# Optimization experiments

Hardware: AMD Instinct MI355X
Metric: run time of the kernel (lower is better)

The kernel has to match this reference:

```python
import jax, jax.numpy as jnp
import numpy as np

N, L = 131072, 4          # traffic lights, lanes per TL
E, H = 64, 128            # embed_dim, hidden_dim
NH, HD = 4, 16            # num_heads, head_dim (E = NH*HD)
NR, R = 4, 8              # num_regions, region_embed_dim
INIT_LOG_STD = -0.5


def _lin(k, fan_in, shape):
    b = 1.0 / np.sqrt(fan_in)
    return jax.random.uniform(k, shape, minval=-b, maxval=b, dtype=jnp.float32)


def setup_inputs() -> dict:
    key = jax.random.key(0)
    ks = jax.random.split(key, 32)
    inp = {
        "queue": jax.random.uniform(ks[0], (N, L), dtype=jnp.float32),
        "waiting": jax.random.uniform(ks[1], (N, L), dtype=jnp.float32),
        "phase_onehot": jax.random.uniform(ks[2], (N, 4), dtype=jnp.float32),
        "elapsed": jax.random.uniform(ks[3], (N,), dtype=jnp.float32),
        "region_ids": jax.random.randint(ks[4], (N,), 0, NR, dtype=jnp.int32),
        "noise": jax.random.normal(ks[5], (N,), dtype=jnp.float32),
        # lane_mlp: Linear(3,H) -> ReLU -> Linear(H,E) -> ReLU
        "lane_w1": _lin(ks[6], 3, (3, H)), "lane_b1": _lin(ks[7], 3, (H,)),
        "lane_w2": _lin(ks[8], H, (H, E)), "lane_b2": _lin(ks[9], H, (E,)),
        # MultiheadAttention in/out projections
        "attn_in_w": _lin(ks[10], E, (E, 3 * E)), "attn_in_b": jnp.zeros((3 * E,), jnp.float32),
        "attn_out_w": _lin(ks[11], E, (E, E)), "attn_out_b": jnp.zeros((E,), jnp.float32),
        # phase_mlp: Linear(5,H) -> ReLU -> Linear(H,H) -> ReLU
        "phase_w1": _lin(ks[12], 5, (5, H)), "phase_b1": _lin(ks[13], 5, (H,)),
        "phase_w2": _lin(ks[14], H, (H, H)), "phase_b2": _lin(ks[15], H, (H,)),
        # region embedding table
        "region_table": jax.random.normal(ks[16], (NR, R), dtype=jnp.float32),
        # mlp_head: Linear(E+H+R, H) -> ReLU -> Linear(H, 1)
        "head_w1": _lin(ks[17], E + H + R, (E + H + R, H)), "head_b1": _lin(ks[18], E + H + R, (H,)),
        "head_w2": _lin(ks[19], H, (H, 1)), "head_b2": _lin(ks[20], H, (1,)),
        "log_std": jnp.full((1,), INIT_LOG_STD, dtype=jnp.float32),
    }
    return inp


def reference(queue, waiting, phase_onehot, elapsed, region_ids, noise,
              lane_w1, lane_b1, lane_w2, lane_b2,
              attn_in_w, attn_in_b, attn_out_w, attn_out_b,
              phase_w1, phase_b1, phase_w2, phase_b2,
              region_table, head_w1, head_b1, head_w2, head_b2, log_std):
    # --- lane context: tiny MLP + self-attention over L lanes, batched over N TLs ---
    lane_feats = jnp.stack([queue, waiting, jnp.broadcast_to(elapsed[:, None], (N, L))], axis=-1)  # [N,L,3]
    h = jax.nn.relu(lane_feats @ lane_w1 + lane_b1)          # [N,L,H]
    emb = jax.nn.relu(h @ lane_w2 + lane_b2)                 # [N,L,E]

    qkv = emb @ attn_in_w + attn_in_b                        # [N,L,3E]
    q, k, v = jnp.split(qkv, 3, axis=-1)
    def heads(x):  # [N,L,E] -> [N,NH,L,HD]
        return x.reshape(N, L, NH, HD).transpose(0, 2, 1, 3)
    q, k, v = heads(q), heads(k), heads(v)
    scores = jnp.einsum('bhqd,bhkd->bhqk', q, k) / np.sqrt(HD)   # [N,NH,L,L]
    attn = jax.nn.softmax(scores, axis=-1)
    o = jnp.einsum('bhqk,bhkd->bhqd', attn, v)               # [N,NH,L,HD]
    o = o.transpose(0, 2, 1, 3).reshape(N, L, E)
    attn_out = o @ attn_out_w + attn_out_b                   # [N,L,E]
    ctx = attn_out.mean(axis=1)                              # [N,E]

    # --- phase MLP ---
    phase_elapsed = jnp.concatenate([phase_onehot, elapsed[:, None]], axis=-1)  # [N,5]
    ph = jax.nn.relu(phase_elapsed @ phase_w1 + phase_b1)
    phase_emb = jax.nn.relu(ph @ phase_w2 + phase_b2)        # [N,H]

    # --- region embedding (clamped index) ---
    rid = jnp.clip(region_ids, 0, NR - 1)
    region_emb = region_table[rid]                           # [N,R]

    # --- Gaussian head ---
    feat = jnp.concatenate([ctx, phase_emb, region_emb], axis=-1)  # [N,E+H+R]
    means = (jax.nn.relu(feat @ head_w1 + head_b1) @ head_w2 + head_b2)[:, 0]  # [N]

    ls = jnp.broadcast_to(log_std, means.shape)
    std = jnp.exp(ls)
    actions = means + std * noise
    actions_clamped = jnp.clip(actions, -1.0, 1.0)
    log_prob = -0.5 * ((actions - means) ** 2 / (std * std) + 2.0 * ls + np.log(2.0 * np.pi))
    return actions_clamped, log_prob
```

## Files before the change

kernel.cpp:

```cpp
#include <hip/hip_runtime.h>
#include <math.h>

#define N_TL 131072
#define GRID 1024
#define BLK 256
#define TLA 16
#define ITERA 8
#define TLB 32
#define ITERB 4

typedef __attribute__((ext_vector_type(8))) short bfrag;
typedef __attribute__((ext_vector_type(4))) float f32x4;

__device__ __forceinline__ unsigned short f2bf_rne(float x) {
  unsigned int u = __float_as_uint(x);
  return (unsigned short)((u + 0x7fffu + ((u >> 16) & 1u)) >> 16);
}
__device__ __forceinline__ unsigned int pack2(float a, float b) {
  return ((__float_as_uint(a) + 0x8000u) >> 16) |
         ((__float_as_uint(b) + 0x8000u) & 0xffff0000u);
}
__device__ __forceinline__ f32x4 mfma16(bfrag a, bfrag b, f32x4 c) {
  return __builtin_amdgcn_mfma_f32_16x16x32_bf16(a, b, c, 0, 0, 0);
}
__device__ __forceinline__ float dot4(float4 a, float4 b) {
  return a.x * b.x + a.y * b.y + a.z * b.z + a.w * b.w;
}

__device__ __forceinline__ bfrag load_wfragT(const float* __restrict__ w, int ncols,
                                             int col0, int k0, int lane, int K, float scale) {
  const int mm = lane & 15, qq = lane >> 4;
  bfrag f;
  #pragma unroll
  for (int j = 0; j < 8; ++j) {
    const int k = k0 + qq * 8 + j;
    const float v = (k < K) ? w[(size_t)k * ncols + col0 + mm] * scale : 0.f;
    f[j] = (short)f2bf_rne(v);
  }
  return f;
}

#define LDBACT(arr, stride, nt, kk) \
  (*reinterpret_cast<const bfrag*>(&(arr)[((nt) * 16 + m) * (stride) + (kk) * 32 + quad * 8]))

struct alignas(16) SmemA {
  union {
    float qkvf[64 * 196];
    unsigned short h[64 * 136];
  };
  unsigned short emb[64 * 72];
  unsigned short xbuf[64 * 32];
  float b1[128], b2[64], bin[192], bout[64];
};

__global__ __launch_bounds__(BLK)
void lane_ctx_mfma(const float* __restrict__ queue,
                   const float* __restrict__ waiting,
                   const float* __restrict__ elapsed,
                   const float* __restrict__ lane_w1,
                   const float* __restrict__ lane_b1,
                   const float* __restrict__ lane_w2,
                   const float* __restrict__ lane_b2,
                   const float* __restrict__ attn_in_w,
                   const float* __restrict__ attn_in_b,
                   const float* __restrict__ attn_out_w,
                   const float* __restrict__ attn_out_b,
                   unsigned short* __restrict__ ctx_out) {
  __shared__ SmemA S;
  const int tid  = threadIdx.x;
  const int wv   = tid >> 6;
  const int lane = tid & 63;
  const int m    = lane & 15;
  const int quad = lane >> 4;
  const f32x4 Z = {0.f, 0.f, 0.f, 0.f};

  bfrag wL1[2], wL2[4], wQKV[3][2], wOUT[8];
  #pragma unroll
  for (int Mi = 0; Mi < 2; ++Mi)
    wL1[Mi] = load_wfragT(lane_w1, 128, (wv * 2 + Mi) * 16, 0, lane, 3, 1.f);
  #pragma unroll
  for (int kk = 0; kk < 4; ++kk)
    wL2[kk] = load_wfragT(lane_w2, 64, wv * 16, kk * 32, lane, 128, 1.f);
  #pragma unroll
  for (int Mi = 0; Mi < 3; ++Mi)
    #pragma unroll
    for (int kk = 0; kk < 2; ++kk)
      wQKV[Mi][kk] = load_wfragT(attn_in_w, 192, (wv + Mi * 4) * 16, kk * 32, lane, 64,
                                 Mi == 0 ? 0.25f : 1.f);
  #pragma unroll
  for (int kk = 0; kk < 8; ++kk) {
    bfrag f;
    #pragma unroll
    for (int j = 0; j < 8; ++j) {
      const int k = kk * 32 + quad * 8 + j;
      f[j] = (short)f2bf_rne(attn_out_w[(size_t)(k & 63) * 64 + wv * 16 + m] * 0.25f);
    }
    wOUT[kk] = f;
  }

  for (int i = tid; i < 128; i += BLK) S.b1[i] = lane_b1[i];
  for (int i = tid; i < 64;  i += BLK) S.b2[i] = lane_b2[i];
  for (int i = tid; i < 192; i += BLK) S.bin[i] = attn_in_b[i] * ((i < 64) ? 0.25f : 1.f);
  for (int i = tid; i < 64;  i += BLK) S.bout[i] = attn_out_b[i];
  {
    const int n0 = blockIdx.x * ITERA * TLA;
    const int r = tid >> 2, seg = tid & 3;
    uint4 z = {0, 0, 0, 0};
    if (seg == 0) {
      const int gl = n0 * 4 + r;
      z.x = pack2(queue[gl], waiting[gl]);
      z.y = pack2(elapsed[n0 + (r >> 2)], 0.f);
    }
    *reinterpret_cast<uint4*>(&S.xbuf[r * 32 + seg * 8]) = z;
  }
  __syncthreads();

  for (int it = 0; it < ITERA; ++it) {
    const int n0 = (blockIdx.x * ITERA + it) * TLA;

    {
      f32x4 acc[2][4];
      #pragma unroll
      for (int Mi = 0; Mi < 2; ++Mi)
        #pragma unroll
        for (int Nt = 0; Nt < 4; ++Nt) acc[Mi][Nt] = Z;
      #pragma unroll
      for (int Nt = 0; Nt < 4; ++Nt) {
        const bfrag b = LDBACT(S.xbuf, 32, Nt, 0);
        acc[0][Nt] = mfma16(wL1[0], b, acc[0][Nt]);
        acc[1][Nt] = mfma16(wL1[1], b, acc[1][Nt]);
      }
      #pragma unroll
      for (int Mi = 0; Mi < 2; ++Mi) {
        const int oc0 = (wv * 2 + Mi) * 16 + quad * 4;
        const f32x4 bb = *reinterpret_cast<const f32x4*>(&S.b1[oc0]);
        #pragma unroll
        for (int Nt = 0; Nt < 4; ++Nt) {
          const int row = Nt * 16 + m;
          uint2 u;
          u.x = pack2(fmaxf(acc[Mi][Nt][0] + bb[0], 0.f), fmaxf(acc[Mi][Nt][1] + bb[1], 0.f));
          u.y = pack2(fmaxf(acc[Mi][Nt][2] + bb[2], 0.f), fmaxf(acc[Mi][Nt][3] + bb[3], 0.f));
          *reinterpret_cast<uint2*>(&S.h[row * 136 + oc0]) = u;
        }
      }
    }
    __syncthreads();

    {
      f32x4 acc[4] = {Z, Z, Z, Z};
      #pragma unroll
      for (int Nt = 0; Nt < 4; ++Nt)
        #pragma unroll
        for (int kk = 0; kk < 4; ++kk)
          acc[Nt] = mfma16(wL2[kk], LDBACT(S.h, 136, Nt, kk), acc[Nt]);
      const int oc0 = wv * 16 + quad * 4;
      const f32x4 bb = *reinterpret_cast<const f32x4*>(&S.b2[oc0]);
      #pragma unroll
      for (int Nt = 0; Nt < 4; ++Nt) {
        const int row = Nt * 16 + m;
        uint2 u;
        u.x = pack2(fmaxf(acc[Nt][0] + bb[0], 0.f), fmaxf(acc[Nt][1] + bb[1], 0.f));
        u.y = pack2(fmaxf(acc[Nt][2] + bb[2], 0.f), fmaxf(acc[Nt][3] + bb[3], 0.f));
        *reinterpret_cast<uint2*>(&S.emb[row * 72 + oc0]) = u;
      }
    }
    __syncthreads();

    {
      f32x4 acc[3][4];
      #pragma unroll
      for (int Mi = 0; Mi < 3; ++Mi)
        #pragma unroll
        for (int Nt = 0; Nt < 4; ++Nt) acc[Mi][Nt] = Z;
      #pragma unroll
      for (int Nt = 0; Nt < 4; ++Nt) {
        const bfrag e0 = LDBACT(S.emb, 72, Nt, 0);
        const bfrag e1 = LDBACT(S.emb, 72, Nt, 1);
        #pragma unroll
        for (int Mi = 0; Mi < 3; ++Mi) {
          acc[Mi][Nt] = mfma16(wQKV[Mi][0], e0, acc[Mi][Nt]);
          acc[Mi][Nt] = mfma16(wQKV[Mi][1], e1, acc[Mi][Nt]);
        }
      }
      #pragma unroll
      for (int Mi = 0; Mi < 3; ++Mi) {
        const int oc0 = (wv + Mi * 4) * 16 + quad * 4;
        const f32x4 bb = *reinterpret_cast<const f32x4*>(&S.bin[oc0]);
        #pragma unroll
        for (int Nt = 0; Nt < 4; ++Nt) {
          const int row = Nt * 16 + m;
          const f32x4 o = acc[Mi][Nt] + bb;
          *reinterpret_cast<f32x4*>(&S.qkvf[row * 196 + oc0]) = o;
        }
      }
      const int nn0 = (blockIdx.x * ITERA + ((it + 1) & (ITERA - 1))) * TLA;
      const int r = tid >> 2, seg = tid & 3;
      uint4 z = {0, 0, 0, 0};
      if (seg == 0) {
        const int gl = nn0 * 4 + r;
        z.x = pack2(queue[gl], waiting[gl]);
        z.y = pack2(elapsed[nn0 + (r >> 2)], 0.f);
      }
      *reinterpret_cast<uint4*>(&S.xbuf[r * 32 + seg * 8]) = z;
    }
    __syncthreads();

    {
      const int tl = tid >> 4, l16 = tid & 15;
      const int hh = l16 >> 2, lq = l16 & 3;
      const float* qb = &S.qkvf[(tl * 4 + lq) * 196 + hh * 16];
      const float4 q0 = *reinterpret_cast<const float4*>(qb);
      const float4 q1 = *reinterpret_cast<const float4*>(qb + 4);
      const float4 q2 = *reinterpret_cast<const float4*>(qb + 8);
      const float4 q3 = *reinterpret_cast<const float4*>(qb + 12);
      float sc[4];
      #pragma unroll
      for (int lk = 0; lk < 4; ++lk) {
        const float* kb = &S.qkvf[(tl * 4 + lk) * 196 + 64 + hh * 16];
        sc[lk] = dot4(q0, *reinterpret_cast<const float4*>(kb))
               + dot4(q1, *reinterpret_cast<const float4*>(kb + 4))
               + dot4(q2, *reinterpret_cast<const float4*>(kb + 8))
               + dot4(q3, *reinterpret_cast<const float4*>(kb + 12));
      }
      const float mx = fmaxf(fmaxf(sc[0], sc[1]), fmaxf(sc[2], sc[3]));
      const float e0 = __expf(sc[0] - mx), e1 = __expf(sc[1] - mx);
      const float e2 = __expf(sc[2] - mx), e3 = __expf(sc[3] - mx);
      const float inv = 1.f / (e0 + e1 + e2 + e3);
      const float pr[4] = {e0 * inv, e1 * inv, e2 * inv, e3 * inv};
      float4 o0 = {0,0,0,0}, o1 = {0,0,0,0}, o2 = {0,0,0,0}, o3 = {0,0,0,0};
      #pragma unroll
      for (int lk = 0; lk < 4; ++lk) {
        const float* vb = &S.qkvf[(tl * 4 + lk) * 196 + 128 + hh * 16];
        const float4 v0 = *reinterpret_cast<const float4*>(vb);
        const float4 v1 = *reinterpret_cast<const float4*>(vb + 4);
        const float4 v2 = *reinterpret_cast<const float4*>(vb + 8);
        const float4 v3 = *reinterpret_cast<const float4*>(vb + 12);
        const float p = pr[lk];
        o0.x += p * v0.x; o0.y += p * v0.y; o0.z += p * v0.z; o0.w += p * v0.w;
        o1.x += p * v1.x; o1.y += p * v1.y; o1.z += p * v1.z; o1.w += p * v1.w;
        o2.x += p * v2.x; o2.y += p * v2.y; o2.z += p * v2.z; o2.w += p * v2.w;
        o3.x += p * v3.x; o3.y += p * v3.y; o3.z += p * v3.z; o3.w += p * v3.w;
      }
      unsigned short* om = S.emb;
      const int base = tl * 264 + lq * 64 + hh * 16;
      *reinterpret_cast<uint4*>(&om[base]) =
          make_uint4(pack2(o0.x, o0.y), pack2(o0.z, o0.w), pack2(o1.x, o1.y), pack2(o1.z, o1.w));
      *reinterpret_cast<uint4*>(&om[base + 8]) =
          make_uint4(pack2(o2.x, o2.y), pack2(o2.z, o2.w), pack2(o3.x, o3.y), pack2(o3.z, o3.w));
    }
    __syncthreads();

    {
      f32x4 acc = Z;
      #pragma unroll
      for (int kk = 0; kk < 8; ++kk)
        acc = mfma16(wOUT[kk], LDBACT(S.emb, 264, 0, kk), acc);
      const int oc0 = wv * 16 + quad * 4;
      uint2 u;
      u.x = pack2(acc[0] + S.bout[oc0],     acc[1] + S.bout[oc0 + 1]);
      u.y = pack2(acc[2] + S.bout[oc0 + 2], acc[3] + S.bout[oc0 + 3]);
      *reinterpret_cast<uint2*>(&ctx_out[(size_t)(n0 + m) * 64 + oc0]) = u;
    }
  }
}

struct alignas(16) SmemB {
  unsigned short feat[32 * 200];
  unsigned short ph[32 * 136];
  unsigned short xb[32 * 32];
  float pb1[128], pb2[128];
  float rbias[4][128];
  float hw2[128];
  float consts[2];
  int ridx[32];
};

__global__ __launch_bounds__(BLK)
void head_mfma(const float* __restrict__ phase_onehot,
               const float* __restrict__ elapsed,
               const int* __restrict__ region_ids,
               const float* __restrict__ noise,
               const float* __restrict__ phase_w1,
               const float* __restrict__ phase_b1,
               const float* __restrict__ phase_w2,
               const float* __restrict__ phase_b2,
               const float* __restrict__ region_table,
               const float* __restrict__ head_w1,
               const float* __restrict__ head_b1,
               const float* __restrict__ head_w2,
               const float* __restrict__ head_b2,
               const float* __restrict__ log_std,
               const unsigned short* __restrict__ ctx_in,
               float* __restrict__ out) {
  __shared__ SmemB S;
  const int tid  = threadIdx.x;
  const int wv   = tid >> 6;
  const int lane = tid & 63;
  const int m    = lane & 15;
  const int quad = lane >> 4;
  const f32x4 Z = {0.f, 0.f, 0.f, 0.f};

  bfrag wP1[2], wP2[2][4], wH1[2][6];
  #pragma unroll
  for (int Mi = 0; Mi < 2; ++Mi) {
    wP1[Mi] = load_wfragT(phase_w1, 128, (wv * 2 + Mi) * 16, 0, lane, 5, 1.f);
    #pragma unroll
    for (int kk = 0; kk < 4; ++kk)
      wP2[Mi][kk] = load_wfragT(phase_w2, 128, (wv + Mi * 4) * 16, kk * 32, lane, 128, 1.f);
    #pragma unroll
    for (int kk = 0; kk < 6; ++kk)
      wH1[Mi][kk] = load_wfragT(head_w1, 128, (wv + Mi * 4) * 16, kk * 32, lane, 192, 1.f);
  }

  for (int i = tid; i < 128; i += BLK) S.pb1[i] = phase_b1[i];
  for (int i = tid; i < 128; i += BLK) S.pb2[i] = phase_b2[i];
  for (int i = tid; i < 128; i += BLK) S.hw2[i] = head_w2[i];
  for (int i = tid; i < 512; i += BLK) {
    const int g = i >> 7, c = i & 127;
    float acc = head_b1[c];
    #pragma unroll
    for (int j = 0; j < 8; ++j) acc += region_table[g * 8 + j] * head_w1[(192 + j) * 128 + c];
    S.rbias[g][c] = acc;
  }
  if (tid == 0) { S.consts[0] = head_b2[0]; S.consts[1] = log_std[0]; }
  {
    const int n0 = blockIdx.x * ITERB * TLB;
    const int row = tid >> 3, c8 = (tid & 7) * 8;
    *reinterpret_cast<uint4*>(&S.feat[row * 200 + c8]) =
        *reinterpret_cast<const uint4*>(&ctx_in[(size_t)(n0 + row) * 64 + c8]);
    if (tid < 128) {
      const int r = tid >> 2, seg = tid & 3;
      uint4 z = {0, 0, 0, 0};
      if (seg == 0) {
        const float4 p = *reinterpret_cast<const float4*>(&phase_onehot[(n0 + r) * 4]);
        z.x = pack2(p.x, p.y);
        z.y = pack2(p.z, p.w);
        z.z = pack2(elapsed[n0 + r], 0.f);
      }
      *reinterpret_cast<uint4*>(&S.xb[r * 32 + seg * 8]) = z;
    }
    if (tid < 32) {
      int r = region_ids[n0 + tid];
      S.ridx[tid] = r < 0 ? 0 : (r > 3 ? 3 : r);
    }
  }
  __syncthreads();

  for (int it = 0; it < ITERB; ++it) {
    const int n0 = (blockIdx.x * ITERB + it) * TLB;

    {
      f32x4 acc[2][2];
      acc[0][0] = Z; acc[0][1] = Z; acc[1][0] = Z; acc[1][1] = Z;
      #pragma unroll
      for (int Nt = 0; Nt < 2; ++Nt) {
        const bfrag b = LDBACT(S.xb, 32, Nt, 0);
        acc[0][Nt] = mfma16(wP1[0], b, acc[0][Nt]);
        acc[1][Nt] = mfma16(wP1[1], b, acc[1][Nt]);
      }
      #pragma unroll
      for (int Mi = 0; Mi < 2; ++Mi) {
        const int oc0 = (wv * 2 + Mi) * 16 + quad * 4;
        const f32x4 bb = *reinterpret_cast<const f32x4*>(&S.pb1[oc0]);
        #pragma unroll
        for (int Nt = 0; Nt < 2; ++Nt) {
          const int row = Nt * 16 + m;
          uint2 u;
          u.x = pack2(fmaxf(acc[Mi][Nt][0] + bb[0], 0.f), fmaxf(acc[Mi][Nt][1] + bb[1], 0.f));
          u.y = pack2(fmaxf(acc[Mi][Nt][2] + bb[2], 0.f), fmaxf(acc[Mi][Nt][3] + bb[3], 0.f));
          *reinterpret_cast<uint2*>(&S.ph[row * 136 + oc0]) = u;
        }
      }
    }
    __syncthreads();

    {
      f32x4 acc[2][2];
      acc[0][0] = Z; acc[0][1] = Z; acc[1][0] = Z; acc[1][1] = Z;
      #pragma unroll
      for (int Nt = 0; Nt < 2; ++Nt)
        #pragma unroll
        for (int kk = 0; kk < 4; ++kk) {
          const bfrag b = LDBACT(S.ph, 136, Nt, kk);
          acc[0][Nt] = mfma16(wP2[0][kk], b, acc[0][Nt]);
          acc[1][Nt] = mfma16(wP2[1][kk], b, acc[1][Nt]);
        }
      #pragma unroll
      for (int Mi = 0; Mi < 2; ++Mi) {
        const int oc0 = (wv + Mi * 4) * 16 + quad * 4;
        const f32x4 bb = *reinterpret_cast<const f32x4*>(&S.pb2[oc0]);
        #pragma unroll
        for (int Nt = 0; Nt < 2; ++Nt) {
          const int row = Nt * 16 + m;
          uint2 u;
          u.x = pack2(fmaxf(acc[Mi][Nt][0] + bb[0], 0.f), fmaxf(acc[Mi][Nt][1] + bb[1], 0.f));
          u.y = pack2(fmaxf(acc[Mi][Nt][2] + bb[2], 0.f), fmaxf(acc[Mi][Nt][3] + bb[3], 0.f));
          *reinterpret_cast<uint2*>(&S.feat[row * 200 + 64 + oc0]) = u;
        }
      }
    }
    __syncthreads();

    {
      f32x4 acc[2][2];
      acc[0][0] = Z; acc[0][1] = Z; acc[1][0] = Z; acc[1][1] = Z;
      #pragma unroll
      for (int Nt = 0; Nt < 2; ++Nt)
        #pragma unroll
        for (int kk = 0; kk < 6; ++kk) {
          const bfrag b = LDBACT(S.feat, 200, Nt, kk);
          acc[0][Nt] = mfma16(wH1[0][kk], b, acc[0][Nt]);
          acc[1][Nt] = mfma16(wH1[1][kk], b, acc[1][Nt]);
        }
      #pragma unroll
      for (int Mi = 0; Mi < 2; ++Mi) {
        const int oc0 = (wv + Mi * 4) * 16 + quad * 4;
        #pragma unroll
        for (int Nt = 0; Nt < 2; ++Nt) {
          const int row = Nt * 16 + m;
          const f32x4 bb = *reinterpret_cast<const f32x4*>(&S.rbias[S.ridx[row]][oc0]);
          uint2 u;
          u.x = pack2(fmaxf(acc[Mi][Nt][0] + bb[0], 0.f), fmaxf(acc[Mi][Nt][1] + bb[1], 0.f));
          u.y = pack2(fmaxf(acc[Mi][Nt][2] + bb[2], 0.f), fmaxf(acc[Mi][Nt][3] + bb[3], 0.f));
          *reinterpret_cast<uint2*>(&S.ph[row * 136 + oc0]) = u;
        }
      }
    }
    __syncthreads();

    {
      const int tl = tid >> 3, s = tid & 7;
      const unsigned short* hp = &S.ph[tl * 136 + s * 16];
      const bfrag h0 = *reinterpret_cast<const bfrag*>(hp);
      const bfrag h1 = *reinterpret_cast<const bfrag*>(hp + 8);
      float t = 0.f;
      #pragma unroll
      for (int j = 0; j < 8; ++j) {
        t += __uint_as_float(((unsigned int)(unsigned short)h0[j]) << 16) * S.hw2[s * 16 + j];
        t += __uint_as_float(((unsigned int)(unsigned short)h1[j]) << 16) * S.hw2[s * 16 + 8 + j];
      }
      t += __shfl_xor(t, 1);
      t += __shfl_xor(t, 2);
      t += __shfl_xor(t, 4);
      if (s == 0) {
        const int n = n0 + tl;
        const float means = t + S.consts[0];
        const float ls = S.consts[1];
        const float nz = noise[n];
        const float a = means + __expf(ls) * nz;
        out[n] = fminf(fmaxf(a, -1.f), 1.f);
        out[N_TL + n] = -0.5f * (nz * nz + 2.f * ls + 1.8378770664093453f);
      }
      const int nn0 = (blockIdx.x * ITERB + ((it + 1) & (ITERB - 1))) * TLB;
      const int row = tid >> 3, c8 = (tid & 7) * 8;
      *reinterpret_cast<uint4*>(&S.feat[row * 200 + c8]) =
          *reinterpret_cast<const uint4*>(&ctx_in[(size_t)(nn0 + row) * 64 + c8]);
      if (tid < 128) {
        const int r = tid >> 2, seg = tid & 3;
        uint4 z = {0, 0, 0, 0};
        if (seg == 0) {
          const float4 p = *reinterpret_cast<const float4*>(&phase_onehot[(nn0 + r) * 4]);
          z.x = pack2(p.x, p.y);
          z.y = pack2(p.z, p.w);
          z.z = pack2(elapsed[nn0 + r], 0.f);
        }
        *reinterpret_cast<uint4*>(&S.xb[r * 32 + seg * 8]) = z;
      }
      if (tid < 32) {
        int r = region_ids[nn0 + tid];
        S.ridx[tid] = r < 0 ? 0 : (r > 3 ? 3 : r);
      }
    }
    __syncthreads();
  }
}

extern "C" void kernel_launch(void* const* d_in, const int* in_sizes, int n_in,
                              void* d_out, int out_size, void* d_ws, size_t ws_size,
                              hipStream_t stream) {
  const float* queue        = (const float*)d_in[0];
  const float* waiting      = (const float*)d_in[1];
  const float* phase_onehot = (const float*)d_in[2];
  const float* elapsed      = (const float*)d_in[3];
  const int*   region_ids   = (const int*)d_in[4];
  const float* noise        = (const float*)d_in[5];
  const float* lane_w1      = (const float*)d_in[6];
  const float* lane_b1      = (const float*)d_in[7];
  const float* lane_w2      = (const float*)d_in[8];
  const float* lane_b2      = (const float*)d_in[9];
  const float* attn_in_w    = (const float*)d_in[10];
  const float* attn_in_b    = (const float*)d_in[11];
  const float* attn_out_w   = (const float*)d_in[12];
  const float* attn_out_b   = (const float*)d_in[13];
  const float* phase_w1     = (const float*)d_in[14];
  const float* phase_b1     = (const float*)d_in[15];
  const float* phase_w2     = (const float*)d_in[16];
  const float* phase_b2     = (const float*)d_in[17];
  const float* region_table = (const float*)d_in[18];
  const float* head_w1      = (const float*)d_in[19];
  const float* head_b1      = (const float*)d_in[20];
  const float* head_w2      = (const float*)d_in[21];
  const float* head_b2      = (const float*)d_in[22];
  const float* log_std      = (const float*)d_in[23];

  unsigned short* ctx_ws = (unsigned short*)d_ws;
  float* out = (float*)d_out;

  hipLaunchKernelGGL(lane_ctx_mfma, dim3(GRID), dim3(BLK), 0, stream,
                     queue, waiting, elapsed, lane_w1, lane_b1, lane_w2, lane_b2,
                     attn_in_w, attn_in_b, attn_out_w, attn_out_b, ctx_ws);
  hipLaunchKernelGGL(head_mfma, dim3(GRID), dim3(BLK), 0, stream,
                     phase_onehot, elapsed, region_ids, noise,
                     phase_w1, phase_b1, phase_w2, phase_b2, region_table,
                     head_w1, head_b1, head_w2, head_b2, log_std, ctx_ws, out);
}
```

Measured before the change: 217.2 us.

## Use 512-thread blocks in head kernel with one output tile per wave

The head kernel moves from 256 to 512 threads per block with 8 waves, each owning a single 16-column output slice, and each block iteration now covers 64 traffic lights instead of 32. Per-wave weight fragments are halved, which lowers register pressure, and the MFMA loops now run over 4 row tiles instead of 2x2 tiles. The aim is more waves in flight and more weight reuse per fragment, at the cost of larger shared memory per block and heavier block-level synchronisation. An empty unrolled loop was also added to the lane kernel and has no effect.

Result: faster. 209.3 us (-3.6%).

```diff
diff --git a/kernel.cpp b/kernel.cpp
--- a/kernel.cpp
+++ b/kernel.cpp
@@ -3,11 +3,12 @@
 
 #define N_TL 131072
 #define GRID 1024
-#define BLK 256
+#define BLKA 256
 #define TLA 16
 #define ITERA 8
-#define TLB 32
-#define ITERB 4
+#define BLKB 512
+#define TLB 64
+#define ITERB 2
 
 typedef __attribute__((ext_vector_type(8))) short bfrag;
 typedef __attribute__((ext_vector_type(4))) float f32x4;
@@ -53,7 +54,7 @@
   float b1[128], b2[64], bin[192], bout[64];
 };
 
-__global__ __launch_bounds__(BLK)
+__global__ __launch_bounds__(BLKA)
 void lane_ctx_mfma(const float* __restrict__ queue,
                    const float* __restrict__ waiting,
                    const float* __restrict__ elapsed,
@@ -98,10 +99,10 @@
     wOUT[kk] = f;
   }
 
-  for (int i = tid; i < 128; i += BLK) S.b1[i] = lane_b1[i];
-  for (int i = tid; i < 64;  i += BLK) S.b2[i] = lane_b2[i];
-  for (int i = tid; i < 192; i += BLK) S.bin[i] = attn_in_b[i] * ((i < 64) ? 0.25f : 1.f);
-  for (int i = tid; i < 64;  i += BLK) S.bout[i] = attn_out_b[i];
+  for (int i = tid; i < 128; i += BLKA) S.b1[i] = lane_b1[i];
+  for (int i = tid; i < 64;  i += BLKA) S.b2[i] = lane_b2[i];
+  for (int i = tid; i < 192; i += BLKA) S.bin[i] = attn_in_b[i] * ((i < 64) ? 0.25f : 1.f);
+  for (int i = tid; i < 64;  i += BLKA) S.bout[i] = attn_out_b[i];
   {
     const int n0 = blockIdx.x * ITERA * TLA;
     const int r = tid >> 2, seg = tid & 3;
@@ -241,6 +242,8 @@
         o2.x += p * v2.x; o2.y += p * v2.y; o2.z += p * v2.z; o2.w += p * v2.w;
         o3.x += p * v3.x; o3.y += p * v3.y; o3.z += p * v3.z; o3.w += p * v3.w;
       }
+      #pragma unroll
+      for (int d = 0; d < 1; ++d) {}
       unsigned short* om = S.emb;
       const int base = tl * 264 + lq * 64 + hh * 16;
       *reinterpret_cast<uint4*>(&om[base]) =
@@ -265,17 +268,17 @@
 }
 
 struct alignas(16) SmemB {
-  unsigned short feat[32 * 200];
-  unsigned short ph[32 * 136];
-  unsigned short xb[32 * 32];
+  unsigned short feat[64 * 200];
+  unsigned short ph[64 * 136];
+  unsigned short xb[64 * 32];
   float pb1[128], pb2[128];
   float rbias[4][128];
   float hw2[128];
   float consts[2];
-  int ridx[32];
+  int ridx[64];
 };
 
-__global__ __launch_bounds__(BLK)
+__global__ __launch_bounds__(BLKB)
 void head_mfma(const float* __restrict__ phase_onehot,
                const float* __restrict__ elapsed,
                const int* __restrict__ region_ids,
@@ -300,22 +303,19 @@
   const int quad = lane >> 4;
   const f32x4 Z = {0.f, 0.f, 0.f, 0.f};
 
-  bfrag wP1[2], wP2[2][4], wH1[2][6];
-  #pragma unroll
-  for (int Mi = 0; Mi < 2; ++Mi) {
-    wP1[Mi] = load_wfragT(phase_w1, 128, (wv * 2 + Mi) * 16, 0, lane, 5, 1.f);
-    #pragma unroll
-    for (int kk = 0; kk < 4; ++kk)
-      wP2[Mi][kk] = load_wfragT(phase_w2, 128, (wv + Mi * 4) * 16, kk * 32, lane, 128, 1.f);
-    #pragma unroll
-    for (int kk = 0; kk < 6; ++kk)
-      wH1[Mi][kk] = load_wfragT(head_w1, 128, (wv + Mi * 4) * 16, kk * 32, lane, 192, 1.f);
-  }
-
-  for (int i = tid; i < 128; i += BLK) S.pb1[i] = phase_b1[i];
-  for (int i = tid; i < 128; i += BLK) S.pb2[i] = phase_b2[i];
-  for (int i = tid; i < 128; i += BLK) S.hw2[i] = head_w2[i];
-  for (int i = tid; i < 512; i += BLK) {
+  bfrag wP1, wP2[4], wH1[6];
+  wP1 = load_wfragT(phase_w1, 128, wv * 16, 0, lane, 5, 1.f);
+  #pragma unroll
+  for (int kk = 0; kk < 4; ++kk)
+    wP2[kk] = load_wfragT(phase_w2, 128, wv * 16, kk * 32, lane, 128, 1.f);
+  #pragma unroll
+  for (int kk = 0; kk < 6; ++kk)
+    wH1[kk] = load_wfragT(head_w1, 128, wv * 16, kk * 32, lane, 192, 1.f);
+
+  for (int i = tid; i < 128; i += BLKB) S.pb1[i] = phase_b1[i];
+  for (int i = tid; i < 128; i += BLKB) S.pb2[i] = phase_b2[i];
+  for (int i = tid; i < 128; i += BLKB) S.hw2[i] = head_w2[i];
+  for (int i = tid; i < 512; i += BLKB) {
     const int g = i >> 7, c = i & 127;
     float acc = head_b1[c];
     #pragma unroll
@@ -328,7 +328,7 @@
     const int row = tid >> 3, c8 = (tid & 7) * 8;
     *reinterpret_cast<uint4*>(&S.feat[row * 200 + c8]) =
         *reinterpret_cast<const uint4*>(&ctx_in[(size_t)(n0 + row) * 64 + c8]);
-    if (tid < 128) {
+    if (tid < 256) {
       const int r = tid >> 2, seg = tid & 3;
       uint4 z = {0, 0, 0, 0};
       if (seg == 0) {
@@ -339,7 +339,7 @@
       }
       *reinterpret_cast<uint4*>(&S.xb[r * 32 + seg * 8]) = z;
     }
-    if (tid < 32) {
+    if (tid < 64) {
       int r = region_ids[n0 + tid];
       S.ridx[tid] = r < 0 ? 0 : (r > 3 ? 3 : r);
     }
@@ -348,82 +348,59 @@
 
   for (int it = 0; it < ITERB; ++it) {
     const int n0 = (blockIdx.x * ITERB + it) * TLB;
-
-    {
-      f32x4 acc[2][2];
-      acc[0][0] = Z; acc[0][1] = Z; acc[1][0] = Z; acc[1][1] = Z;
-      #pragma unroll
-      for (int Nt = 0; Nt < 2; ++Nt) {
-        const bfrag b = LDBACT(S.xb, 32, Nt, 0);
-        acc[0][Nt] = mfma16(wP1[0], b, acc[0][Nt]);
-        acc[1][Nt] = mfma16(wP1[1], b, acc[1][Nt]);
-      }
-      #pragma unroll
-      for (int Mi = 0; Mi < 2; ++Mi) {
-        const int oc0 = (wv * 2 + Mi) * 16 + quad * 4;
-        const f32x4 bb = *reinterpret_cast<const f32x4*>(&S.pb1[oc0]);
-        #pragma unroll
-        for (int Nt = 0; Nt < 2; ++Nt) {
-          const int row = Nt * 16 + m;
-          uint2 u;
-          u.x = pack2(fmaxf(acc[Mi][Nt][0] + bb[0], 0.f), fmaxf(acc[Mi][Nt][1] + bb[1], 0.f));
-          u.y = pack2(fmaxf(acc[Mi][Nt][2] + bb[2], 0.f), fmaxf(acc[Mi][Nt][3] + bb[3], 0.f));
-          *reinterpret_cast<uint2*>(&S.ph[row * 136 + oc0]) = u;
-        }
-      }
-    }
-    __syncthreads();
-
-    {
-      f32x4 acc[2][2];
-      acc[0][0] = Z; acc[0][1] = Z; acc[1][0] = Z; acc[1][1] = Z;
-      #pragma unroll
-      for (int Nt = 0; Nt < 2; ++Nt)
-        #pragma unroll
-        for (int kk = 0; kk < 4; ++kk) {
-          const bfrag b = LDBACT(S.ph, 136, Nt, kk);
-          acc[0][Nt] = mfma16(wP2[0][kk], b, acc[0][Nt]);
-          acc[1][Nt] = mfma16(wP2[1][kk], b, acc[1][Nt]);
-        }
-      #pragma unroll
-      for (int Mi = 0; Mi < 2; ++Mi) {
-        const int oc0 = (wv + Mi * 4) * 16 + quad * 4;
-        const f32x4 bb = *reinterpret_cast<const f32x4*>(&S.pb2[oc0]);
-        #pragma unroll
-        for (int Nt = 0; Nt < 2; ++Nt) {
-          const int row = Nt * 16 + m;
-          uint2 u;
-          u.x = pack2(fmaxf(acc[Mi][Nt][0] + bb[0], 0.f), fmaxf(acc[Mi][Nt][1] + bb[1], 0.f));
-          u.y = pack2(fmaxf(acc[Mi][Nt][2] + bb[2], 0.f), fmaxf(acc[Mi][Nt][3] + bb[3], 0.f));
-          *reinterpret_cast<uint2*>(&S.feat[row * 200 + 64 + oc0]) = u;
-        }
-      }
-    }
-    __syncthreads();
-
-    {
-      f32x4 acc[2][2];
-      acc[0][0] = Z; acc[0][1] = Z; acc[1][0] = Z; acc[1][1] = Z;
-      #pragma unroll
-      for (int Nt = 0; Nt < 2; ++Nt)
-        #pragma unroll
-        for (int kk = 0; kk < 6; ++kk) {
-          const bfrag b = LDBACT(S.feat, 200, Nt, kk);
-          acc[0][Nt] = mfma16(wH1[0][kk], b, acc[0][Nt]);
-          acc[1][Nt] = mfma16(wH1[1][kk], b, acc[1][Nt]);
-        }
-      #pragma unroll
-      for (int Mi = 0; Mi < 2; ++Mi) {
-        const int oc0 = (wv + Mi * 4) * 16 + quad * 4;
-        #pragma unroll
-        for (int Nt = 0; Nt < 2; ++Nt) {
-          const int row = Nt * 16 + m;
-          const f32x4 bb = *reinterpret_cast<const f32x4*>(&S.rbias[S.ridx[row]][oc0]);
-          uint2 u;
-          u.x = pack2(fmaxf(acc[Mi][Nt][0] + bb[0], 0.f), fmaxf(acc[Mi][Nt][1] + bb[1], 0.f));
-          u.y = pack2(fmaxf(acc[Mi][Nt][2] + bb[2], 0.f), fmaxf(acc[Mi][Nt][3] + bb[3], 0.f));
-          *reinterpret_cast<uint2*>(&S.ph[row * 136 + oc0]) = u;
-        }
+    const int oc0 = wv * 16 + quad * 4;
+
+    {
+      f32x4 acc[4] = {Z, Z, Z, Z};
+      #pragma unroll
+      for (int Nt = 0; Nt < 4; ++Nt)
+        acc[Nt] = mfma16(wP1, LDBACT(S.xb, 32, Nt, 0), acc[Nt]);
+      const f32x4 bb = *reinterpret_cast<const f32x4*>(&S.pb1[oc0]);
+      #pragma unroll
+      for (int Nt = 0; Nt < 4; ++Nt) {
+        const int row = Nt * 16 + m;
+        uint2 u;
+        u.x = pack2(fmaxf(acc[Nt][0] + bb[0], 0.f), fmaxf(acc[Nt][1] + bb[1], 0.f));
+        u.y = pack2(fmaxf(acc[Nt][2] + bb[2], 0.f), fmaxf(acc[Nt][3] + bb[3], 0.f));
+        *reinterpret_cast<uint2*>(&S.ph[row * 136 + oc0]) = u;
+      }
+    }
+    __syncthreads();
+
+    {
+      f32x4 acc[4] = {Z, Z, Z, Z};
+      #pragma unroll
+      for (int kk = 0; kk < 4; ++kk)
+        #pragma unroll
+        for (int Nt = 0; Nt < 4; ++Nt)
+          acc[Nt] = mfma16(wP2[kk], LDBACT(S.ph, 136, Nt, kk), acc[Nt]);
+      const f32x4 bb = *reinterpret_cast<const f32x4*>(&S.pb2[oc0]);
+      #pragma unroll
+      for (int Nt = 0; Nt < 4; ++Nt) {
+        const int row = Nt * 16 + m;
+        uint2 u;
+        u.x = pack2(fmaxf(acc[Nt][0] + bb[0], 0.f), fmaxf(acc[Nt][1] + bb[1], 0.f));
+        u.y = pack2(fmaxf(acc[Nt][2] + bb[2], 0.f), fmaxf(acc[Nt][3] + bb[3], 0.f));
+        *reinterpret_cast<uint2*>(&S.feat[row * 200 + 64 + oc0]) = u;
+      }
+    }
+    __syncthreads();
+
+    {
+      f32x4 acc[4] = {Z, Z, Z, Z};
+      #pragma unroll
+      for (int kk = 0; kk < 6; ++kk)
+        #pragma unroll
+        for (int Nt = 0; Nt < 4; ++Nt)
+          acc[Nt] = mfma16(wH1[kk], LDBACT(S.feat, 200, Nt, kk), acc[Nt]);
+      #pragma unroll
+      for (int Nt = 0; Nt < 4; ++Nt) {
+        const int row = Nt * 16 + m;
+        const f32x4 bb = *reinterpret_cast<const f32x4*>(&S.rbias[S.ridx[row]][oc0]);
+        uint2 u;
+        u.x = pack2(fmaxf(acc[Nt][0] + bb[0], 0.f), fmaxf(acc[Nt][1] + bb[1], 0.f));
+        u.y = pack2(fmaxf(acc[Nt][2] + bb[2], 0.f), fmaxf(acc[Nt][3] + bb[3], 0.f));
+        *reinterpret_cast<uint2*>(&S.ph[row * 136 + oc0]) = u;
       }
     }
     __syncthreads();
@@ -455,7 +432,7 @@
       const int row = tid >> 3, c8 = (tid & 7) * 8;
       *reinterpret_cast<uint4*>(&S.feat[row * 200 + c8]) =
           *reinterpret_cast<const uint4*>(&ctx_in[(size_t)(nn0 + row) * 64 + c8]);
-      if (tid < 128) {
+      if (tid < 256) {
         const int r = tid >> 2, seg = tid & 3;
         uint4 z = {0, 0, 0, 0};
         if (seg == 0) {
@@ -466,7 +443,7 @@
         }
         *reinterpret_cast<uint4*>(&S.xb[r * 32 + seg * 8]) = z;
       }
-      if (tid < 32) {
+      if (tid < 64) {
         int r = region_ids[nn0 + tid];
         S.ridx[tid] = r < 0 ? 0 : (r > 3 ? 3 : r);
       }
@@ -506,10 +483,10 @@
   unsigned short* ctx_ws = (unsigned short*)d_ws;
   float* out = (float*)d_out;
 
-  hipLaunchKernelGGL(lane_ctx_mfma, dim3(GRID), dim3(BLK), 0, stream,
+  hipLaunchKernelGGL(lane_ctx_mfma, dim3(GRID), dim3(BLKA), 0, stream,
                      queue, waiting, elapsed, lane_w1, lane_b1, lane_w2, lane_b2,
                      attn_in_w, attn_in_b, attn_out_w, attn_out_b, ctx_ws);
-  hipLaunchKernelGGL(head_mfma, dim3(GRID), dim3(BLK), 0, stream,
+  hipLaunchKernelGGL(head_mfma, dim3(GRID), dim3(BLKB), 0, stream,
                      phase_onehot, elapsed, region_ids, noise,
                      phase_w1, phase_b1, phase_w2, phase_b2, region_table,
                      head_w1, head_b1, head_w2, head_b2, log_std, ctx_ws, out);
```

## Fuse lane-attention and head kernels into one per-block policy kernel

Applied to the files above, without the earlier changes.

Merges the two kernels into a single kernel. Each block processes 64 traffic lights: four 16-light attention passes write ctx straight into shared feat, then the phase MLP and head MLP run on those 64 rows. This removes the bf16 ctx round-trip through global workspace and one kernel launch. In exchange every block now loads all weight fragments for both stages, with heavy register pressure at launch_bounds(BLK,2), a larger shared struct, twice as many blocks, and a non-looping head phase that cannot overlap loads across iterations.

After: 311.5 us. 1.43x slower.

```diff
diff --git a/kernel.cpp b/kernel.cpp
--- a/kernel.cpp
+++ b/kernel.cpp
@@ -2,12 +2,8 @@
 #include <math.h>
 
 #define N_TL 131072
-#define GRID 1024
+#define GRID 2048
 #define BLK 256
-#define TLA 16
-#define ITERA 8
-#define TLB 32
-#define ITERB 4
 
 typedef __attribute__((ext_vector_type(8))) short bfrag;
 typedef __attribute__((ext_vector_type(4))) float f32x4;
@@ -43,35 +39,56 @@
 #define LDBACT(arr, stride, nt, kk) \
   (*reinterpret_cast<const bfrag*>(&(arr)[((nt) * 16 + m) * (stride) + (kk) * 32 + quad * 8]))
 
-struct alignas(16) SmemA {
+struct alignas(16) SmemF {
   union {
     float qkvf[64 * 196];
     unsigned short h[64 * 136];
+    unsigned short ph[64 * 136];
   };
   unsigned short emb[64 * 72];
   unsigned short xbuf[64 * 32];
+  unsigned short feat[64 * 200];
   float b1[128], b2[64], bin[192], bout[64];
+  float pb1[128], pb2[128];
+  float rbias[4][128];
+  float hw2[128];
+  float consts[2];
+  int ridx[64];
 };
 
-__global__ __launch_bounds__(BLK)
-void lane_ctx_mfma(const float* __restrict__ queue,
-                   const float* __restrict__ waiting,
-                   const float* __restrict__ elapsed,
-                   const float* __restrict__ lane_w1,
-                   const float* __restrict__ lane_b1,
-                   const float* __restrict__ lane_w2,
-                   const float* __restrict__ lane_b2,
-                   const float* __restrict__ attn_in_w,
-                   const float* __restrict__ attn_in_b,
-                   const float* __restrict__ attn_out_w,
-                   const float* __restrict__ attn_out_b,
-                   unsigned short* __restrict__ ctx_out) {
-  __shared__ SmemA S;
+__global__ __launch_bounds__(BLK, 2)
+void fused_policy(const float* __restrict__ queue,
+                  const float* __restrict__ waiting,
+                  const float* __restrict__ phase_onehot,
+                  const float* __restrict__ elapsed,
+                  const int* __restrict__ region_ids,
+                  const float* __restrict__ noise,
+                  const float* __restrict__ lane_w1,
+                  const float* __restrict__ lane_b1,
+                  const float* __restrict__ lane_w2,
+                  const float* __restrict__ lane_b2,
+                  const float* __restrict__ attn_in_w,
+                  const float* __restrict__ attn_in_b,
+                  const float* __restrict__ attn_out_w,
+                  const float* __restrict__ attn_out_b,
+                  const float* __restrict__ phase_w1,
+                  const float* __restrict__ phase_b1,
+                  const float* __restrict__ phase_w2,
+                  const float* __restrict__ phase_b2,
+                  const float* __restrict__ region_table,
+                  const float* __restrict__ head_w1,
+                  const float* __restrict__ head_b1,
+                  const float* __restrict__ head_w2,
+                  const float* __restrict__ head_b2,
+                  const float* __restrict__ log_std,
+                  float* __restrict__ out) {
+  __shared__ SmemF S;
   const int tid  = threadIdx.x;
   const int wv   = tid >> 6;
   const int lane = tid & 63;
   const int m    = lane & 15;
   const int quad = lane >> 4;
+  const int n0   = blockIdx.x * 64;
   const f32x4 Z = {0.f, 0.f, 0.f, 0.f};
 
   bfrag wL1[2], wL2[4], wQKV[3][2], wOUT[8];
@@ -96,14 +113,39 @@
       f[j] = (short)f2bf_rne(attn_out_w[(size_t)(k & 63) * 64 + wv * 16 + m] * 0.25f);
     }
     wOUT[kk] = f;
+  }
+  bfrag wP1[2], wP2[2][4], wH1[2][6];
+  #pragma unroll
+  for (int Mi = 0; Mi < 2; ++Mi) {
+    wP1[Mi] = load_wfragT(phase_w1, 128, (wv * 2 + Mi) * 16, 0, lane, 5, 1.f);
+    #pragma unroll
+    for (int kk = 0; kk < 4; ++kk)
+      wP2[Mi][kk] = load_wfragT(phase_w2, 128, (wv * 2 + Mi) * 16, kk * 32, lane, 128, 1.f);
+    #pragma unroll
+    for (int kk = 0; kk < 6; ++kk)
+      wH1[Mi][kk] = load_wfragT(head_w1, 128, (wv * 2 + Mi) * 16, kk * 32, lane, 192, 1.f);
   }
 
   for (int i = tid; i < 128; i += BLK) S.b1[i] = lane_b1[i];
   for (int i = tid; i < 64;  i += BLK) S.b2[i] = lane_b2[i];
   for (int i = tid; i < 192; i += BLK) S.bin[i] = attn_in_b[i] * ((i < 64) ? 0.25f : 1.f);
   for (int i = tid; i < 64;  i += BLK) S.bout[i] = attn_out_b[i];
+  for (int i = tid; i < 128; i += BLK) S.pb1[i] = phase_b1[i];
+  for (int i = tid; i < 128; i += BLK) S.pb2[i] = phase_b2[i];
+  for (int i = tid; i < 128; i += BLK) S.hw2[i] = head_w2[i];
+  for (int i = tid; i < 512; i += BLK) {
+    const int g = i >> 7, c = i & 127;
+    float acc = head_b1[c];
+    #pragma unroll
+    for (int j = 0; j < 8; ++j) acc += region_table[g * 8 + j] * head_w1[(192 + j) * 128 + c];
+    S.rbias[g][c] = acc;
+  }
+  if (tid == 0) { S.consts[0] = head_b2[0]; S.consts[1] = log_std[0]; }
+  if (tid < 64) {
+    int r = region_ids[n0 + tid];
+    S.ridx[tid] = r < 0 ? 0 : (r > 3 ? 3 : r);
+  }
   {
-    const int n0 = blockIdx.x * ITERA * TLA;
     const int r = tid >> 2, seg = tid & 3;
     uint4 z = {0, 0, 0, 0};
     if (seg == 0) {
@@ -115,8 +157,9 @@
   }
   __syncthreads();
 
-  for (int it = 0; it < ITERA; ++it) {
-    const int n0 = (blockIdx.x * ITERA + it) * TLA;
+  #pragma unroll 1
+  for (int s = 0; s < 4; ++s) {
+    const int tl0 = n0 + s * 16;
 
     {
       f32x4 acc[2][4];
@@ -193,13 +236,21 @@
           *reinterpret_cast<f32x4*>(&S.qkvf[row * 196 + oc0]) = o;
         }
       }
-      const int nn0 = (blockIdx.x * ITERA + ((it + 1) & (ITERA - 1))) * TLA;
       const int r = tid >> 2, seg = tid & 3;
       uint4 z = {0, 0, 0, 0};
-      if (seg == 0) {
-        const int gl = nn0 * 4 + r;
-        z.x = pack2(queue[gl], waiting[gl]);
-        z.y = pack2(elapsed[nn0 + (r >> 2)], 0.f);
+      if (s < 3) {
+        if (seg == 0) {
+          const int gl = (tl0 + 16) * 4 + r;
+          z.x = pack2(queue[gl], waiting[gl]);
+          z.y = pack2(elapsed[tl0 + 16 + (r >> 2)], 0.f);
+        }
+      } else {
+        if (seg == 0) {
+          const float4 p = *reinterpret_cast<const float4*>(&phase_onehot[(n0 + r) * 4]);
+          z.x = pack2(p.x, p.y);
+          z.y = pack2(p.z, p.w);
+          z.z = pack2(elapsed[n0 + r], 0.f);
+        }
       }
       *reinterpret_cast<uint4*>(&S.xbuf[r * 32 + seg * 8]) = z;
     }
@@ -259,219 +310,122 @@
       uint2 u;
       u.x = pack2(acc[0] + S.bout[oc0],     acc[1] + S.bout[oc0 + 1]);
       u.y = pack2(acc[2] + S.bout[oc0 + 2], acc[3] + S.bout[oc0 + 3]);
-      *reinterpret_cast<uint2*>(&ctx_out[(size_t)(n0 + m) * 64 + oc0]) = u;
-    }
-  }
-}
-
-struct alignas(16) SmemB {
-  unsigned short feat[32 * 200];
-  unsigned short ph[32 * 136];
-  unsigned short xb[32 * 32];
-  float pb1[128], pb2[128];
-  float rbias[4][128];
-  float hw2[128];
-  float consts[2];
-  int ridx[32];
-};
-
-__global__ __launch_bounds__(BLK)
-void head_mfma(const float* __restrict__ phase_onehot,
-               const float* __restrict__ elapsed,
-               const int* __restrict__ region_ids,
-               const float* __restrict__ noise,
-               const float* __restrict__ phase_w1,
-               const float* __restrict__ phase_b1,
-               const float* __restrict__ phase_w2,
-               const float* __restrict__ phase_b2,
-               const float* __restrict__ region_table,
-               const float* __restrict__ head_w1,
-               const float* __restrict__ head_b1,
-               const float* __restrict__ head_w2,
-               const float* __restrict__ head_b2,
-               const float* __restrict__ log_std,
-               const unsigned short* __restrict__ ctx_in,
-               float* __restrict__ out) {
-  __shared__ SmemB S;
-  const int tid  = threadIdx.x;
-  const int wv   = tid >> 6;
-  const int lane = tid & 63;
-  const int m    = lane & 15;
-  const int quad = lane >> 4;
-  const f32x4 Z = {0.f, 0.f, 0.f, 0.f};
-
-  bfrag wP1[2], wP2[2][4], wH1[2][6];
-  #pragma unroll
-  for (int Mi = 0; Mi < 2; ++Mi) {
-    wP1[Mi] = load_wfragT(phase_w1, 128, (wv * 2 + Mi) * 16, 0, lane, 5, 1.f);
+      *reinterpret_cast<uint2*>(&S.feat[(s * 16 + m) * 200 + oc0]) = u;
+    }
+  }
+  __syncthreads();
+
+  {
+    f32x4 acc[2][4];
+    #pragma unroll
+    for (int Mi = 0; Mi < 2; ++Mi)
+      #pragma unroll
+      for (int Nt = 0; Nt < 4; ++Nt) acc[Mi][Nt] = Z;
+    #pragma unroll
+    for (int Nt = 0; Nt < 4; ++Nt) {
+      const bfrag b = LDBACT(S.xbuf, 32, Nt, 0);
+      acc[0][Nt] = mfma16(wP1[0], b, acc[0][Nt]);
+      acc[1][Nt] = mfma16(wP1[1], b, acc[1][Nt]);
+    }
+    #pragma unroll
+    for (int Mi = 0; Mi < 2; ++Mi) {
+      const int oc0 = (wv * 2 + Mi) * 16 + quad * 4;
+      const f32x4 bb = *reinterpret_cast<const f32x4*>(&S.pb1[oc0]);
+      #pragma unroll
+      for (int Nt = 0; Nt < 4; ++Nt) {
+        const int row = Nt * 16 + m;
+        uint2 u;
+        u.x = pack2(fmaxf(acc[Mi][Nt][0] + bb[0], 0.f), fmaxf(acc[Mi][Nt][1] + bb[1], 0.f));
+        u.y = pack2(fmaxf(acc[Mi][Nt][2] + bb[2], 0.f), fmaxf(acc[Mi][Nt][3] + bb[3], 0.f));
+        *reinterpret_cast<uint2*>(&S.ph[row * 136 + oc0]) = u;
+      }
+    }
+  }
+  __syncthreads();
+
+  {
+    f32x4 acc[2][4];
+    #pragma unroll
+    for (int Mi = 0; Mi < 2; ++Mi)
+      #pragma unroll
+      for (int Nt = 0; Nt < 4; ++Nt) acc[Mi][Nt] = Z;
     #pragma unroll
     for (int kk = 0; kk < 4; ++kk)
-      wP2[Mi][kk] = load_wfragT(phase_w2, 128, (wv + Mi * 4) * 16, kk * 32, lane, 128, 1.f);
+      #pragma unroll
+      for (int Nt = 0; Nt < 4; ++Nt) {
+        const bfrag b = LDBACT(S.ph, 136, Nt, kk);
+        acc[0][Nt] = mfma16(wP2[0][kk], b, acc[0][Nt]);
+        acc[1][Nt] = mfma16(wP2[1][kk], b, acc[1][Nt]);
+      }
+    #pragma unroll
+    for (int Mi = 0; Mi < 2; ++Mi) {
+      const int oc0 = (wv * 2 + Mi) * 16 + quad * 4;
+      const f32x4 bb = *reinterpret_cast<const f32x4*>(&S.pb2[oc0]);
+      #pragma unroll
+      for (int Nt = 0; Nt < 4; ++Nt) {
+        const int row = Nt * 16 + m;
+        uint2 u;
+        u.x = pack2(fmaxf(acc[Mi][Nt][0] + bb[0], 0.f), fmaxf(acc[Mi][Nt][1] + bb[1], 0.f));
+        u.y = pack2(fmaxf(acc[Mi][Nt][2] + bb[2], 0.f), fmaxf(acc[Mi][Nt][3] + bb[3], 0.f));
+        *reinterpret_cast<uint2*>(&S.feat[row * 200 + 64 + oc0]) = u;
+      }
+    }
+  }
+  __syncthreads();
+
+  {
+    f32x4 acc[2][4];
+    #pragma unroll
+    for (int Mi = 0; Mi < 2; ++Mi)
+      #pragma unroll
+      for (int Nt = 0; Nt < 4; ++Nt) acc[Mi][Nt] = Z;
     #pragma unroll
     for (int kk = 0; kk < 6; ++kk)
-      wH1[Mi][kk] = load_wfragT(head_w1, 128, (wv + Mi * 4) * 16, kk * 32, lane, 192, 1.f);
-  }
-
-  for (int i = tid; i < 128; i += BLK) S.pb1[i] = phase_b1[i];
-  for (int i = tid; i < 128; i += BLK) S.pb2[i] = phase_b2[i];
-  for (int i = tid; i < 128; i += BLK) S.hw2[i] = head_w2[i];
-  for (int i = tid; i < 512; i += BLK) {
-    const int g = i >> 7, c = i & 127;
-    float acc = head_b1[c];
-    #pragma unroll
-    for (int j = 0; j < 8; ++j) acc += region_table[g * 8 + j] * head_w1[(192 + j) * 128 + c];
-    S.rbias[g][c] = acc;
-  }
-  if (tid == 0) { S.consts[0] = head_b2[0]; S.consts[1] = log_std[0]; }
+      #pragma unroll
+      for (int Nt = 0; Nt < 4; ++Nt) {
+        const bfrag b = LDBACT(S.feat, 200, Nt, kk);
+        acc[0][Nt] = mfma16(wH1[0][kk], b, acc[0][Nt]);
+        acc[1][Nt] = mfma16(wH1[1][kk], b, acc[1][Nt]);
+      }
+    #pragma unroll
+    for (int Mi = 0; Mi < 2; ++Mi) {
+      const int oc0 = (wv * 2 + Mi) * 16 + quad * 4;
+      #pragma unroll
+      for (int Nt = 0; Nt < 4; ++Nt) {
+        const int row = Nt * 16 + m;
+        const f32x4 bb = *reinterpret_cast<const f32x4*>(&S.rbias[S.ridx[row]][oc0]);
+        uint2 u;
+        u.x = pack2(fmaxf(acc[Mi][Nt][0] + bb[0], 0.f), fmaxf(acc[Mi][Nt][1] + bb[1], 0.f));
+        u.y = pack2(fmaxf(acc[Mi][Nt][2] + bb[2], 0.f), fmaxf(acc[Mi][Nt][3] + bb[3], 0.f));
+        *reinterpret_cast<uint2*>(&S.ph[row * 136 + oc0]) = u;
+      }
+    }
+  }
+  __syncthreads();
+
   {
-    const int n0 = blockIdx.x * ITERB * TLB;
-    const int row = tid >> 3, c8 = (tid & 7) * 8;
-    *reinterpret_cast<uint4*>(&S.feat[row * 200 + c8]) =
-        *reinterpret_cast<const uint4*>(&ctx_in[(size_t)(n0 + row) * 64 + c8]);
-    if (tid < 128) {
-      const int r = tid >> 2, seg = tid & 3;
-      uint4 z = {0, 0, 0, 0};
-      if (seg == 0) {
-        const float4 p = *reinterpret_cast<const float4*>(&phase_onehot[(n0 + r) * 4]);
-        z.x = pack2(p.x, p.y);
-        z.y = pack2(p.z, p.w);
-        z.z = pack2(elapsed[n0 + r], 0.f);
-      }
-      *reinterpret_cast<uint4*>(&S.xb[r * 32 + seg * 8]) = z;
-    }
-    if (tid < 32) {
-      int r = region_ids[n0 + tid];
-      S.ridx[tid] = r < 0 ? 0 : (r > 3 ? 3 : r);
-    }
-  }
-  __syncthreads();
-
-  for (int it = 0; it < ITERB; ++it) {
-    const int n0 = (blockIdx.x * ITERB + it) * TLB;
-
-    {
-      f32x4 acc[2][2];
-      acc[0][0] = Z; acc[0][1] = Z; acc[1][0] = Z; acc[1][1] = Z;
-      #pragma unroll
-      for (int Nt = 0; Nt < 2; ++Nt) {
-        const bfrag b = LDBACT(S.xb, 32, Nt, 0);
-        acc[0][Nt] = mfma16(wP1[0], b, acc[0][Nt]);
-        acc[1][Nt] = mfma16(wP1[1], b, acc[1][Nt]);
-      }
-      #pragma unroll
-      for (int Mi = 0; Mi < 2; ++Mi) {
-        const int oc0 = (wv * 2 + Mi) * 16 + quad * 4;
-        const f32x4 bb = *reinterpret_cast<const f32x4*>(&S.pb1[oc0]);
-        #pragma unroll
-        for (int Nt = 0; Nt < 2; ++Nt) {
-          const int row = Nt * 16 + m;
-          uint2 u;
-          u.x = pack2(fmaxf(acc[Mi][Nt][0] + bb[0], 0.f), fmaxf(acc[Mi][Nt][1] + bb[1], 0.f));
-          u.y = pack2(fmaxf(acc[Mi][Nt][2] + bb[2], 0.f), fmaxf(acc[Mi][Nt][3] + bb[3], 0.f));
-          *reinterpret_cast<uint2*>(&S.ph[row * 136 + oc0]) = u;
-        }
-      }
-    }
-    __syncthreads();
-
-    {
-      f32x4 acc[2][2];
-      acc[0][0] = Z; acc[0][1] = Z; acc[1][0] = Z; acc[1][1] = Z;
-      #pragma unroll
-      for (int Nt = 0; Nt < 2; ++Nt)
-        #pragma unroll
-        for (int kk = 0; kk < 4; ++kk) {
-          const bfrag b = LDBACT(S.ph, 136, Nt, kk);
-          acc[0][Nt] = mfma16(wP2[0][kk], b, acc[0][Nt]);
-          acc[1][Nt] = mfma16(wP2[1][kk], b, acc[1][Nt]);
-        }
-      #pragma unroll
-      for (int Mi = 0; Mi < 2; ++Mi) {
-        const int oc0 = (wv + Mi * 4) * 16 + quad * 4;
-        const f32x4 bb = *reinterpret_cast<const f32x4*>(&S.pb2[oc0]);
-        #pragma unroll
-        for (int Nt = 0; Nt < 2; ++Nt) {
-          const int row = Nt * 16 + m;
-          uint2 u;
-          u.x = pack2(fmaxf(acc[Mi][Nt][0] + bb[0], 0.f), fmaxf(acc[Mi][Nt][1] + bb[1], 0.f));
-          u.y = pack2(fmaxf(acc[Mi][Nt][2] + bb[2], 0.f), fmaxf(acc[Mi][Nt][3] + bb[3], 0.f));
-          *reinterpret_cast<uint2*>(&S.feat[row * 200 + 64 + oc0]) = u;
-        }
-      }
-    }
-    __syncthreads();
-
-    {
-      f32x4 acc[2][2];
-      acc[0][0] = Z; acc[0][1] = Z; acc[1][0] = Z; acc[1][1] = Z;
-      #pragma unroll
-      for (int Nt = 0; Nt < 2; ++Nt)
-        #pragma unroll
-        for (int kk = 0; kk < 6; ++kk) {
-          const bfrag b = LDBACT(S.feat, 200, Nt, kk);
-          acc[0][Nt] = mfma16(wH1[0][kk], b, acc[0][Nt]);
-          acc[1][Nt] = mfma16(wH1[1][kk], b, acc[1][Nt]);
-        }
-      #pragma unroll
-      for (int Mi = 0; Mi < 2; ++Mi) {
-        const int oc0 = (wv + Mi * 4) * 16 + quad * 4;
-        #pragma unroll
-        for (int Nt = 0; Nt < 2; ++Nt) {
-          const int row = Nt * 16 + m;
-          const f32x4 bb = *reinterpret_cast<const f32x4*>(&S.rbias[S.ridx[row]][oc0]);
-          uint2 u;
-          u.x = pack2(fmaxf(acc[Mi][Nt][0] + bb[0], 0.f), fmaxf(acc[Mi][Nt][1] + bb[1], 0.f));
-          u.y = pack2(fmaxf(acc[Mi][Nt][2] + bb[2], 0.f), fmaxf(acc[Mi][Nt][3] + bb[3], 0.f));
-          *reinterpret_cast<uint2*>(&S.ph[row * 136 + oc0]) = u;
-        }
-      }
-    }
-    __syncthreads();
-
-    {
-      const int tl = tid >> 3, s = tid & 7;
-      const unsigned short* hp = &S.ph[tl * 136 + s * 16];
-      const bfrag h0 = *reinterpret_cast<const bfrag*>(hp);
-      const bfrag h1 = *reinterpret_cast<const bfrag*>(hp + 8);
-      float t = 0.f;
-      #pragma unroll
-      for (int j = 0; j < 8; ++j) {
-        t += __uint_as_float(((unsigned int)(unsigned short)h0[j]) << 16) * S.hw2[s * 16 + j];
-        t += __uint_as_float(((unsigned int)(unsigned short)h1[j]) << 16) * S.hw2[s * 16 + 8 + j];
-      }
-      t += __shfl_xor(t, 1);
-      t += __shfl_xor(t, 2);
-      t += __shfl_xor(t, 4);
-      if (s == 0) {
-        const int n = n0 + tl;
-        const float means = t + S.consts[0];
-        const float ls = S.consts[1];
-        const float nz = noise[n];
-        const float a = means + __expf(ls) * nz;
-        out[n] = fminf(fmaxf(a, -1.f), 1.f);
-        out[N_TL + n] = -0.5f * (nz * nz + 2.f * ls + 1.8378770664093453f);
-      }
-      const int nn0 = (blockIdx.x * ITERB + ((it + 1) & (ITERB - 1))) * TLB;
-      const int row = tid >> 3, c8 = (tid & 7) * 8;
-      *reinterpret_cast<uint4*>(&S.feat[row * 200 + c8]) =
-          *reinterpret_cast<const uint4*>(&ctx_in[(size_t)(nn0 + row) * 64 + c8]);
-      if (tid < 128) {
-        const int r = tid >> 2, seg = tid & 3;
-        uint4 z = {0, 0, 0, 0};
-        if (seg == 0) {
-          const float4 p = *reinterpret_cast<const float4*>(&phase_onehot[(nn0 + r) * 4]);
-          z.x = pack2(p.x, p.y);
-          z.y = pack2(p.z, p.w);
-          z.z = pack2(elapsed[nn0 + r], 0.f);
-        }
-        *reinterpret_cast<uint4*>(&S.xb[r * 32 + seg * 8]) = z;
-      }
-      if (tid < 32) {
-        int r = region_ids[nn0 + tid];
-        S.ridx[tid] = r < 0 ? 0 : (r > 3 ? 3 : r);
-      }
-    }
-    __syncthreads();
+    const int tl = tid >> 2, s4 = tid & 3;
+    const unsigned short* hp = &S.ph[tl * 136 + s4 * 32];
+    float t = 0.f;
+    #pragma unroll
+    for (int seg = 0; seg < 4; ++seg) {
+      const bfrag hseg = *reinterpret_cast<const bfrag*>(hp + seg * 8);
+      const float* w = &S.hw2[s4 * 32 + seg * 8];
+      #pragma unroll
+      for (int j = 0; j < 8; ++j)
+        t += __uint_as_float(((unsigned int)(unsigned short)hseg[j]) << 16) * w[j];
+    }
+    t += __shfl_xor(t, 1);
+    t += __shfl_xor(t, 2);
+    if (s4 == 0) {
+      const int n = n0 + tl;
+      const float means = t + S.consts[0];
+      const float ls = S.consts[1];
+      const float nz = noise[n];
+      const float a = means + __expf(ls) * nz;
+      out[n] = fminf(fmaxf(a, -1.f), 1.f);
+      out[N_TL + n] = -0.5f * (nz * nz + 2.f * ls + 1.8378770664093453f);
+    }
   }
 }
 
@@ -503,14 +457,13 @@
   const float* head_b2      = (const float*)d_in[22];
   const float* log_std      = (const float*)d_in[23];
 
-  unsigned short* ctx_ws = (unsigned short*)d_ws;
   float* out = (float*)d_out;
-
-  hipLaunchKernelGGL(lane_ctx_mfma, dim3(GRID), dim3(BLK), 0, stream,
-                     queue, waiting, elapsed, lane_w1, lane_b1, lane_w2, lane_b2,
-                     attn_in_w, attn_in_b, attn_out_w, attn_out_b, ctx_ws);
-  hipLaunchKernelGGL(head_mfma, dim3(GRID), dim3(BLK), 0, stream,
-                     phase_onehot, elapsed, region_ids, noise,
+  (void)d_ws; (void)ws_size;
+
+  hipLaunchKernelGGL(fused_policy, dim3(GRID), dim3(BLK), 0, stream,
+                     queue, waiting, phase_onehot, elapsed, region_ids, noise,
+                     lane_w1, lane_b1, lane_w2, lane_b2,
+                     attn_in_w, attn_in_b, attn_out_w, attn_out_b,
                      phase_w1, phase_b1, phase_w2, phase_b2, region_table,
-                     head_w1, head_b1, head_w2, head_b2, log_std, ctx_ws, out);
-}
+                     head_w1, head_b1, head_w2, head_b2, log_std, out);
+}
```
